# Performance work log

Measured on AMD Instinct MI355X. Metric: run time of the kernel, lower is better.

The kernel has to match this reference:

```python
import jax, jax.numpy as jnp
import numpy as np


def setup_inputs() -> dict:
    key = jax.random.key(0)
    kq, kk, kv = jax.random.split(key, 3)
    B, L, H, E = 4, 2048, 16, 64
    return {
        "queries": jax.random.normal(kq, (B, L, H, E), dtype=jnp.float32),
        "keys": jax.random.normal(kk, (B, L, H, E), dtype=jnp.float32),
        "values": jax.random.normal(kv, (B, L, H, E), dtype=jnp.float32),
    }


def reference(queries, keys, values):
    B, L, H, E = queries.shape
    S = keys.shape[1]
    scale = 1.0 / jnp.sqrt(jnp.asarray(E, queries.dtype))
    # scores: [B, H, L, S]
    scores = jnp.einsum("blhe,bshe->bhls", queries, keys)
    # causal mask: disallow s > l (upper triangle, diagonal=1)
    causal = jnp.triu(jnp.ones((L, S), dtype=bool), k=1)
    scores = jnp.where(causal[None, None], -jnp.inf, scores)
    A = jax.nn.softmax(scale * scores, axis=-1)
    V = jnp.einsum("bhls,bshd->blhd", A, values)
    return V
```

## Files before the change

### kernel.cpp

```cpp
#include <hip/hip_runtime.h>
#include <hip/hip_bf16.h>

typedef __attribute__((ext_vector_type(8))) short short8;
typedef __attribute__((ext_vector_type(4))) float f32x4;
typedef __attribute__((ext_vector_type(4))) float f4;
typedef __attribute__((ext_vector_type(2))) unsigned uint2v;
typedef __attribute__((ext_vector_type(4))) unsigned uint4v;

#define MFMA(a, b, c) __builtin_amdgcn_mfma_f32_16x16x32_bf16(a, b, c, 0, 0, 0)

constexpr int B_ = 4, L = 2048, H = 16, E = 64;
constexpr int QBLK = 128, KVBLK = 64, NW = 8;
constexpr int LDP = 72;
constexpr float LOG2E = 1.4426950408889634f;
constexpr float C2 = 14.426950408889634f;
constexpr size_t NELEM = (size_t)B_ * L * H * E;
constexpr size_t WS_NEEDED = NELEM * 2 * 2;
constexpr int TILE_SHORTS = KVBLK * E;

__device__ __forceinline__ unsigned short f2bf(float f) {
  union { float f; unsigned u; } x;
  x.f = f;
  unsigned r = x.u + 0x7fffu + ((x.u >> 16) & 1u);
  return (unsigned short)(r >> 16);
}

__device__ __forceinline__ float exp2_fast(float x) {
  float r;
  asm("v_exp_f32 %0, %1" : "=v"(r) : "v"(x));
  return r;
}
__device__ __forceinline__ unsigned cvt_pk_bf16(float lo, float hi) {
  unsigned r;
  asm("v_cvt_pk_bf16_f32 %0, %1, %2" : "=v"(r) : "v"(lo), "v"(hi));
  return r;
}

__device__ __forceinline__ void gload_lds16(const void* g, void* l) {
  __builtin_amdgcn_global_load_lds(
      (const __attribute__((address_space(1))) unsigned*)g,
      (__attribute__((address_space(3))) unsigned*)l, 16, 0, 0);
}

__device__ __forceinline__ void stage_tile8(const unsigned short* gtile,
                                            unsigned short* ltile,
                                            unsigned qb, unsigned qs) {
  gload_lds16((const char*)gtile + qs, (char*)ltile + qb);
}

__device__ __forceinline__ void barrier_fence() {
  asm volatile("" ::: "memory");
  __builtin_amdgcn_s_barrier();
  asm volatile("" ::: "memory");
}

__global__ __launch_bounds__(256)
void prep_all(const float* __restrict__ K, const float* __restrict__ V,
              unsigned short* __restrict__ Kb, unsigned short* __restrict__ Vt) {
  __shared__ unsigned short Ts[E][KVBLK + 8];
  const int tid = threadIdx.x;
  if (blockIdx.y == 0) {
    const size_t t = (size_t)blockIdx.x * 256 + tid;
    const size_t row = t >> 3;
    const int e0 = ((int)t & 7) * 8;
    const int h = (int)(row % H);
    const size_t bl = row / H;
    const int l = (int)(bl % L);
    const int b = (int)(bl / L);
    f4 a = *(const f4*)(K + t * 8);
    f4 c = *(const f4*)(K + t * 8 + 4);
    short8 o;
    o[0] = (short)f2bf(a[0]); o[1] = (short)f2bf(a[1]);
    o[2] = (short)f2bf(a[2]); o[3] = (short)f2bf(a[3]);
    o[4] = (short)f2bf(c[0]); o[5] = (short)f2bf(c[1]);
    o[6] = (short)f2bf(c[2]); o[7] = (short)f2bf(c[3]);
    *(short8*)(Kb + (((size_t)b * H + h) * L + l) * E + e0) = o;
    return;
  }
  const int blk = blockIdx.x;
  if (blk >= B_ * H * (L / KVBLK)) return;
  const int st = blk % (L / KVBLK);
  const int bh = blk / (L / KVBLK);
  const int h = bh % H, b = bh / H;
  const int r = tid >> 3, e0 = (tid & 7) * 8;
  const float* vp = V + (((size_t)b * L + st * KVBLK) * H + h) * E;
#pragma unroll
  for (int rr = 0; rr < 2; ++rr) {
    const int row = rr * 32 + r;
    f4 a = *(const f4*)(vp + (size_t)row * (H * E) + e0);
    f4 c = *(const f4*)(vp + (size_t)row * (H * E) + e0 + 4);
#pragma unroll
    for (int j = 0; j < 4; ++j) Ts[e0 + j][row] = f2bf(a[j]);
#pragma unroll
    for (int j = 0; j < 4; ++j) Ts[e0 + 4 + j][row] = f2bf(c[j]);
  }
  __syncthreads();
  const int e = tid >> 2, k0 = (tid & 3) * 16;
  unsigned short* op = Vt + ((size_t)bh * (L / KVBLK) + st) * (E * KVBLK) + e * KVBLK + k0;
  *(short8*)op = *(const short8*)&Ts[e][k0];
  *(short8*)(op + 8) = *(const short8*)&Ts[e][k0 + 8];
}

__global__ __launch_bounds__(512, 6)
void fattn3(const float* __restrict__ Q, const unsigned short* __restrict__ Kb,
            const unsigned short* __restrict__ Vt, float* __restrict__ O) {
  const int bh = blockIdx.x;
  const int qtile = (int)(gridDim.y - 1) - blockIdx.y;
  const int b = bh >> 4, h = bh & 15;
  const int tid = threadIdx.x;
  const int wid = tid >> 6;
  const int lane = tid & 63;
  const int lg = lane >> 4, lm = lane & 15;
  const int qrow0 = qtile * QBLK + wid * 16;

  __shared__ __align__(16) unsigned short Ks[2][TILE_SHORTS];
  __shared__ __align__(16) unsigned short Vs[2][TILE_SHORTS];
  __shared__ __align__(16) unsigned short Pt[NW][16 * LDP];

  const unsigned sqb = (unsigned)wid * 1024u + (unsigned)lane * 16u;
  const unsigned sqs = sqb ^ (((sqb >> 7) & 7u) << 4);

  const unsigned short* kbase = Kb + (size_t)bh * L * E;
  const unsigned short* vbase = Vt + (size_t)bh * L * E;

  stage_tile8(kbase, Ks[0], sqb, sqs);
  stage_tile8(vbase, Vs[0], sqb, sqs);

  int offA[4], offB[4];
#pragma unroll
  for (int ct = 0; ct < 4; ++ct) {
    const int row = ct * 16 + lm;
    offA[ct] = row * 128 + ((lg ^ (row & 7)) << 4);
    offB[ct] = row * 128 + (((4 + lg) ^ (row & 7)) << 4);
  }
  int wrOff[4];
#pragma unroll
  for (int ct = 0; ct < 4; ++ct) wrOff[ct] = (lm * LDP + ct * 16 + lg * 4) * 2;
  const int rdOff0 = (lm * LDP + lg * 8) * 2;
  const int rdOff1 = (lm * LDP + 32 + lg * 8) * 2;
  char* const ptw = (char*)Pt[wid];

  short8 qf0, qf1;
  {
    const float qsc = 0.125f * LOG2E;
    const float* qp = Q + (((size_t)b * L + qrow0 + lm) * H + h) * E + lg * 8;
    f4 a0 = *(const f4*)(qp);
    f4 a1 = *(const f4*)(qp + 4);
    f4 b0 = *(const f4*)(qp + 32);
    f4 b1 = *(const f4*)(qp + 36);
    uint4v u0 = { cvt_pk_bf16(a0[0] * qsc, a0[1] * qsc),
                  cvt_pk_bf16(a0[2] * qsc, a0[3] * qsc),
                  cvt_pk_bf16(a1[0] * qsc, a1[1] * qsc),
                  cvt_pk_bf16(a1[2] * qsc, a1[3] * qsc) };
    uint4v u1 = { cvt_pk_bf16(b0[0] * qsc, b0[1] * qsc),
                  cvt_pk_bf16(b0[2] * qsc, b0[3] * qsc),
                  cvt_pk_bf16(b1[0] * qsc, b1[1] * qsc),
                  cvt_pk_bf16(b1[2] * qsc, b1[3] * qsc) };
    qf0 = __builtin_bit_cast(short8, u0);
    qf1 = __builtin_bit_cast(short8, u1);
  }

  f32x4 o[4];
#pragma unroll
  for (int et = 0; et < 4; ++et) o[et] = (f32x4){0.f, 0.f, 0.f, 0.f};
  float lsum = 0.f;

  const int nkv = 2 * qtile + 2;
  const f32x4 cinit = (f32x4){-C2, -C2, -C2, -C2};

  for (int kt = 0; kt < nkv; ++kt) {
    const int cur = kt & 1, nxt = cur ^ 1;

    asm volatile("s_waitcnt lgkmcnt(0)" ::: "memory");
    barrier_fence();

    if (kt + 1 < nkv) {
      stage_tile8(kbase + (size_t)(kt + 1) * TILE_SHORTS, Ks[nxt], sqb, sqs);
      stage_tile8(vbase + (size_t)(kt + 1) * TILE_SHORTS, Vs[nxt], sqb, sqs);
      asm volatile("s_waitcnt vmcnt(2)" ::: "memory");
    } else {
      asm volatile("s_waitcnt vmcnt(0)" ::: "memory");
    }
    barrier_fence();

    const bool dead = (kt * KVBLK) > (qrow0 + 15);
    if (dead) continue;

    const char* kl = (const char*)Ks[cur];
    const char* vl = (const char*)Vs[cur];

    f32x4 stl[4];
    __builtin_amdgcn_s_setprio(1);
#pragma unroll
    for (int ct = 0; ct < 4; ++ct) {
      short8 k0f = *(const short8*)(kl + offA[ct]);
      short8 k1f = *(const short8*)(kl + offB[ct]);
      f32x4 acc = cinit;
      acc = MFMA(k0f, qf0, acc);
      acc = MFMA(k1f, qf1, acc);
      stl[ct] = acc;
    }
    __builtin_amdgcn_s_setprio(0);

    if (kt * KVBLK + KVBLK - 1 > qrow0) {
#pragma unroll
      for (int ct = 0; ct < 4; ++ct)
#pragma unroll
        for (int r = 0; r < 4; ++r) {
          const int key = kt * KVBLK + ct * 16 + lg * 4 + r;
          if (key > qrow0 + lm) stl[ct][r] = -1e30f;
        }
    }

#pragma unroll
    for (int ct = 0; ct < 4; ++ct)
#pragma unroll
      for (int r = 0; r < 4; ++r) {
        const float p = exp2_fast(stl[ct][r]);
        stl[ct][r] = p;
        lsum += p;
      }

#pragma unroll
    for (int ct = 0; ct < 4; ++ct) {
      uint2v w;
      w[0] = cvt_pk_bf16(stl[ct][0], stl[ct][1]);
      w[1] = cvt_pk_bf16(stl[ct][2], stl[ct][3]);
      *(uint2v*)(ptw + wrOff[ct]) = w;
    }
    short8 pf0 = *(const short8*)(ptw + rdOff0);
    short8 pf1 = *(const short8*)(ptw + rdOff1);

    __builtin_amdgcn_s_setprio(1);
#pragma unroll
    for (int et = 0; et < 4; ++et) {
      short8 v0 = *(const short8*)(vl + offA[et]);
      short8 v1 = *(const short8*)(vl + offB[et]);
      o[et] = MFMA(pf0, v0, o[et]);
      o[et] = MFMA(pf1, v1, o[et]);
    }
    __builtin_amdgcn_s_setprio(0);
  }

  lsum += __shfl_xor(lsum, 16);
  lsum += __shfl_xor(lsum, 32);
  float linv[4];
#pragma unroll
  for (int r = 0; r < 4; ++r) linv[r] = 1.f / __shfl(lsum, lg * 20 + r);
  float* op = O + (((size_t)b * L + qrow0 + lg * 4) * H + h) * E;
#pragma unroll
  for (int r = 0; r < 4; ++r)
#pragma unroll
    for (int et = 0; et < 4; ++et)
      op[(size_t)r * (H * E) + et * 16 + lm] = o[et][r] * linv[r];
}

constexpr int LDV_F = 72, LDP_F = 72;
__global__ __launch_bounds__(256, 2)
void fattn_v1(const float* __restrict__ Q, const float* __restrict__ K,
              const float* __restrict__ V, float* __restrict__ O) {
  const int qtile = blockIdx.x;
  const int bh = blockIdx.y;
  const int b = bh / H, h = bh % H;
  const int tid = threadIdx.x;
  const int wid = tid >> 6;
  const int lane = tid & 63;
  const int lg = lane >> 4, lm = lane & 15;
  __shared__ __align__(16) short Vs[E * LDV_F];
  __shared__ __align__(16) short Ps[4][16 * LDP_F];
  const int qrow0 = qtile * 64 + wid * 16;
  short8 qf[2];
  {
    const float* qp = Q + (((size_t)b * L + (qrow0 + lm)) * H + h) * E + lg * 8;
#pragma unroll
    for (int kc = 0; kc < 2; ++kc) {
      f4 a = *(const f4*)(qp + kc * 32);
      f4 c = *(const f4*)(qp + kc * 32 + 4);
      short8 r;
      r[0] = (short)f2bf(a[0] * 0.125f); r[1] = (short)f2bf(a[1] * 0.125f);
      r[2] = (short)f2bf(a[2] * 0.125f); r[3] = (short)f2bf(a[3] * 0.125f);
      r[4] = (short)f2bf(c[0] * 0.125f); r[5] = (short)f2bf(c[1] * 0.125f);
      r[6] = (short)f2bf(c[2] * 0.125f); r[7] = (short)f2bf(c[3] * 0.125f);
      qf[kc] = r;
    }
  }
  f32x4 o[4];
#pragma unroll
  for (int et = 0; et < 4; ++et) o[et] = (f32x4){0.f, 0.f, 0.f, 0.f};
  float mrow[4], lrow[4];
#pragma unroll
  for (int r = 0; r < 4; ++r) { mrow[r] = -1e30f; lrow[r] = 0.f; }
  const float* kbase = K + (((size_t)b * L) * H + h) * E;
  const float* vbase = V + (((size_t)b * L) * H + h) * E;
  const int nkv = qtile + 1;
  for (int kt = 0; kt < nkv; ++kt) {
    __syncthreads();
    {
      const int key = tid >> 2;
      const int eb = (tid & 3) * 16;
      const float* vp = vbase + (size_t)(kt * 64 + key) * (H * E) + eb;
#pragma unroll
      for (int i = 0; i < 4; ++i) {
        f4 v = *(const f4*)(vp + i * 4);
        Vs[(eb + i * 4 + 0) * LDV_F + key] = (short)f2bf(v[0]);
        Vs[(eb + i * 4 + 1) * LDV_F + key] = (short)f2bf(v[1]);
        Vs[(eb + i * 4 + 2) * LDV_F + key] = (short)f2bf(v[2]);
        Vs[(eb + i * 4 + 3) * LDV_F + key] = (short)f2bf(v[3]);
      }
    }
    f32x4 s[4];
#pragma unroll
    for (int ct = 0; ct < 4; ++ct) {
      f32x4 acc = (f32x4){0.f, 0.f, 0.f, 0.f};
      const float* kp = kbase + (size_t)(kt * 64 + ct * 16 + lm) * (H * E) + lg * 8;
#pragma unroll
      for (int kc = 0; kc < 2; ++kc) {
        f4 a = *(const f4*)(kp + kc * 32);
        f4 c = *(const f4*)(kp + kc * 32 + 4);
        short8 kf;
        kf[0] = (short)f2bf(a[0]); kf[1] = (short)f2bf(a[1]);
        kf[2] = (short)f2bf(a[2]); kf[3] = (short)f2bf(a[3]);
        kf[4] = (short)f2bf(c[0]); kf[5] = (short)f2bf(c[1]);
        kf[6] = (short)f2bf(c[2]); kf[7] = (short)f2bf(c[3]);
        acc = MFMA(qf[kc], kf, acc);
      }
      s[ct] = acc;
    }
    if (kt == nkv - 1) {
#pragma unroll
      for (int ct = 0; ct < 4; ++ct) {
        const int sg = kt * 64 + ct * 16 + lm;
#pragma unroll
        for (int r = 0; r < 4; ++r)
          if (sg > qrow0 + lg * 4 + r) s[ct][r] = -1e30f;
      }
    }
#pragma unroll
    for (int r = 0; r < 4; ++r) {
      float tm = fmaxf(fmaxf(s[0][r], s[1][r]), fmaxf(s[2][r], s[3][r]));
      tm = fmaxf(tm, __shfl_xor(tm, 1));
      tm = fmaxf(tm, __shfl_xor(tm, 2));
      tm = fmaxf(tm, __shfl_xor(tm, 4));
      tm = fmaxf(tm, __shfl_xor(tm, 8));
      const float mnew = fmaxf(mrow[r], tm);
      const float sc = __expf(mrow[r] - mnew);
      mrow[r] = mnew;
      float rs = 0.f;
#pragma unroll
      for (int ct = 0; ct < 4; ++ct) {
        const float p = __expf(s[ct][r] - mnew);
        s[ct][r] = p;
        rs += p;
      }
      rs += __shfl_xor(rs, 1);
      rs += __shfl_xor(rs, 2);
      rs += __shfl_xor(rs, 4);
      rs += __shfl_xor(rs, 8);
      lrow[r] = lrow[r] * sc + rs;
#pragma unroll
      for (int et = 0; et < 4; ++et) o[et][r] *= sc;
    }
#pragma unroll
    for (int ct = 0; ct < 4; ++ct)
#pragma unroll
      for (int r = 0; r < 4; ++r)
        Ps[wid][(lg * 4 + r) * LDP_F + ct * 16 + lm] = (short)f2bf(s[ct][r]);
    __syncthreads();
    short8 pf[2];
    pf[0] = *(const short8*)&Ps[wid][lm * LDP_F + 0 * 32 + lg * 8];
    pf[1] = *(const short8*)&Ps[wid][lm * LDP_F + 1 * 32 + lg * 8];
#pragma unroll
    for (int et = 0; et < 4; ++et)
#pragma unroll
      for (int kc = 0; kc < 2; ++kc) {
        short8 vf = *(const short8*)&Vs[(et * 16 + lm) * LDV_F + kc * 32 + lg * 8];
        o[et] = MFMA(pf[kc], vf, o[et]);
      }
  }
  float* op = O + (((size_t)b * L + qrow0) * H + h) * E;
#pragma unroll
  for (int r = 0; r < 4; ++r) {
    const float inv = 1.f / lrow[r];
#pragma unroll
    for (int et = 0; et < 4; ++et)
      op[(size_t)(lg * 4 + r) * (H * E) + et * 16 + lm] = o[et][r] * inv;
  }
}

extern "C" void kernel_launch(void* const* d_in, const int* in_sizes, int n_in,
                              void* d_out, int out_size, void* d_ws, size_t ws_size,
                              hipStream_t stream) {
  const float* Q = (const float*)d_in[0];
  const float* K = (const float*)d_in[1];
  const float* V = (const float*)d_in[2];
  float* Out = (float*)d_out;
  if (ws_size >= WS_NEEDED) {
    unsigned short* Kb = (unsigned short*)d_ws;
    unsigned short* Vt = Kb + NELEM;
    dim3 gp((unsigned)(NELEM / (256 * 8)), 2);
    prep_all<<<gp, 256, 0, stream>>>(K, V, Kb, Vt);
    dim3 grid(B_ * H, L / QBLK);
    fattn3<<<grid, 512, 0, stream>>>(Q, Kb, Vt, Out);
  } else {
    dim3 grid(L / 64, B_ * H);
    fattn_v1<<<grid, 256, 0, stream>>>(Q, K, V, Out);
  }
}
```

Measured before the change: 68.58 us.

## Rewrite flash attention kernel around 32x32x16 MFMA with register-resident P

Replaces the 16x16x32 MFMA attention kernel (8 waves, 16 query rows each) with a 4-wave kernel where each wave owns 32 query rows and uses 32x32x16 bf16 MFMAs for both QK^T and PV. The softmax probabilities are repacked into the B-operand layout with cross-half-wave shuffles instead of a round trip through per-wave LDS, which removes the P shared buffer. The aim is to raise MFMA efficiency, reuse each K/V fragment across more rows, and cut LDS traffic. In exchange each wave holds more accumulator registers, and there are fewer waves per block to hide latency.

```diff
diff --git a/kernel.cpp b/kernel.cpp
--- a/kernel.cpp
+++ b/kernel.cpp
@@ -2,16 +2,16 @@
 #include <hip/hip_bf16.h>
 
 typedef __attribute__((ext_vector_type(8))) short short8;
+typedef __attribute__((ext_vector_type(16))) float f32x16;
 typedef __attribute__((ext_vector_type(4))) float f32x4;
 typedef __attribute__((ext_vector_type(4))) float f4;
-typedef __attribute__((ext_vector_type(2))) unsigned uint2v;
 typedef __attribute__((ext_vector_type(4))) unsigned uint4v;
 
-#define MFMA(a, b, c) __builtin_amdgcn_mfma_f32_16x16x32_bf16(a, b, c, 0, 0, 0)
+#define MFMA16(a, b, c) __builtin_amdgcn_mfma_f32_16x16x32_bf16(a, b, c, 0, 0, 0)
+#define MFMA32(a, b, c) __builtin_amdgcn_mfma_f32_32x32x16_bf16(a, b, c, 0, 0, 0)
 
 constexpr int B_ = 4, L = 2048, H = 16, E = 64;
-constexpr int QBLK = 128, KVBLK = 64, NW = 8;
-constexpr int LDP = 72;
+constexpr int QBLK = 128, KVBLK = 64;
 constexpr float LOG2E = 1.4426950408889634f;
 constexpr float C2 = 14.426950408889634f;
 constexpr size_t NELEM = (size_t)B_ * L * H * E;
@@ -40,12 +40,6 @@
   __builtin_amdgcn_global_load_lds(
       (const __attribute__((address_space(1))) unsigned*)g,
       (__attribute__((address_space(3))) unsigned*)l, 16, 0, 0);
-}
-
-__device__ __forceinline__ void stage_tile8(const unsigned short* gtile,
-                                            unsigned short* ltile,
-                                            unsigned qb, unsigned qs) {
-  gload_lds16((const char*)gtile + qs, (char*)ltile + qb);
 }
 
 __device__ __forceinline__ void barrier_fence() {
@@ -101,72 +95,66 @@
   *(short8*)(op + 8) = *(const short8*)&Ts[e][k0 + 8];
 }
 
-__global__ __launch_bounds__(512, 6)
-void fattn3(const float* __restrict__ Q, const unsigned short* __restrict__ Kb,
-            const unsigned short* __restrict__ Vt, float* __restrict__ O) {
+__global__ __launch_bounds__(256, 4)
+void fattn32(const float* __restrict__ Q, const unsigned short* __restrict__ Kb,
+             const unsigned short* __restrict__ Vt, float* __restrict__ O) {
   const int bh = blockIdx.x;
   const int qtile = (int)(gridDim.y - 1) - blockIdx.y;
   const int b = bh >> 4, h = bh & 15;
   const int tid = threadIdx.x;
   const int wid = tid >> 6;
   const int lane = tid & 63;
-  const int lg = lane >> 4, lm = lane & 15;
-  const int qrow0 = qtile * QBLK + wid * 16;
+  const int ql = lane & 31;
+  const int hb = lane >> 5;
+  const int qw0 = qtile * QBLK + wid * 32;
+  const int qglob = qw0 + ql;
 
   __shared__ __align__(16) unsigned short Ks[2][TILE_SHORTS];
   __shared__ __align__(16) unsigned short Vs[2][TILE_SHORTS];
-  __shared__ __align__(16) unsigned short Pt[NW][16 * LDP];
-
-  const unsigned sqb = (unsigned)wid * 1024u + (unsigned)lane * 16u;
-  const unsigned sqs = sqb ^ (((sqb >> 7) & 7u) << 4);
+
+  const unsigned sb0 = (unsigned)wid * 2048u + (unsigned)lane * 16u;
+  const unsigned sb1 = sb0 + 1024u;
+  const unsigned ss0 = sb0 ^ (((sb0 >> 7) & 7u) << 4);
+  const unsigned ss1 = sb1 ^ (((sb1 >> 7) & 7u) << 4);
 
   const unsigned short* kbase = Kb + (size_t)bh * L * E;
   const unsigned short* vbase = Vt + (size_t)bh * L * E;
 
-  stage_tile8(kbase, Ks[0], sqb, sqs);
-  stage_tile8(vbase, Vs[0], sqb, sqs);
-
-  int offA[4], offB[4];
-#pragma unroll
-  for (int ct = 0; ct < 4; ++ct) {
-    const int row = ct * 16 + lm;
-    offA[ct] = row * 128 + ((lg ^ (row & 7)) << 4);
-    offB[ct] = row * 128 + (((4 + lg) ^ (row & 7)) << 4);
-  }
-  int wrOff[4];
-#pragma unroll
-  for (int ct = 0; ct < 4; ++ct) wrOff[ct] = (lm * LDP + ct * 16 + lg * 4) * 2;
-  const int rdOff0 = (lm * LDP + lg * 8) * 2;
-  const int rdOff1 = (lm * LDP + 32 + lg * 8) * 2;
-  char* const ptw = (char*)Pt[wid];
-
-  short8 qf0, qf1;
+  gload_lds16((const char*)kbase + ss0, (char*)Ks[0] + sb0);
+  gload_lds16((const char*)kbase + ss1, (char*)Ks[0] + sb1);
+  gload_lds16((const char*)vbase + ss0, (char*)Vs[0] + sb0);
+  gload_lds16((const char*)vbase + ss1, (char*)Vs[0] + sb1);
+
+  const int mq = ql & 7;
+  int off2[2][4];
+#pragma unroll
+  for (int t2 = 0; t2 < 2; ++t2)
+#pragma unroll
+    for (int j = 0; j < 4; ++j)
+      off2[t2][j] = (t2 * 32 + ql) * 128 + (((2 * j + hb) ^ mq) << 4);
+
+  short8 qf[4];
   {
     const float qsc = 0.125f * LOG2E;
-    const float* qp = Q + (((size_t)b * L + qrow0 + lm) * H + h) * E + lg * 8;
-    f4 a0 = *(const f4*)(qp);
-    f4 a1 = *(const f4*)(qp + 4);
-    f4 b0 = *(const f4*)(qp + 32);
-    f4 b1 = *(const f4*)(qp + 36);
-    uint4v u0 = { cvt_pk_bf16(a0[0] * qsc, a0[1] * qsc),
-                  cvt_pk_bf16(a0[2] * qsc, a0[3] * qsc),
-                  cvt_pk_bf16(a1[0] * qsc, a1[1] * qsc),
-                  cvt_pk_bf16(a1[2] * qsc, a1[3] * qsc) };
-    uint4v u1 = { cvt_pk_bf16(b0[0] * qsc, b0[1] * qsc),
-                  cvt_pk_bf16(b0[2] * qsc, b0[3] * qsc),
-                  cvt_pk_bf16(b1[0] * qsc, b1[1] * qsc),
-                  cvt_pk_bf16(b1[2] * qsc, b1[3] * qsc) };
-    qf0 = __builtin_bit_cast(short8, u0);
-    qf1 = __builtin_bit_cast(short8, u1);
-  }
-
-  f32x4 o[4];
-#pragma unroll
-  for (int et = 0; et < 4; ++et) o[et] = (f32x4){0.f, 0.f, 0.f, 0.f};
+    const float* qp = Q + (((size_t)b * L + qglob) * H + h) * E + hb * 8;
+#pragma unroll
+    for (int kc = 0; kc < 4; ++kc) {
+      f4 x0 = *(const f4*)(qp + kc * 16);
+      f4 x1 = *(const f4*)(qp + kc * 16 + 4);
+      uint4v u = { cvt_pk_bf16(x0[0] * qsc, x0[1] * qsc),
+                   cvt_pk_bf16(x0[2] * qsc, x0[3] * qsc),
+                   cvt_pk_bf16(x1[0] * qsc, x1[1] * qsc),
+                   cvt_pk_bf16(x1[2] * qsc, x1[3] * qsc) };
+      qf[kc] = __builtin_bit_cast(short8, u);
+    }
+  }
+
+  f32x16 o0, o1;
+#pragma unroll
+  for (int r = 0; r < 16; ++r) { o0[r] = 0.f; o1[r] = 0.f; }
   float lsum = 0.f;
 
   const int nkv = 2 * qtile + 2;
-  const f32x4 cinit = (f32x4){-C2, -C2, -C2, -C2};
 
   for (int kt = 0; kt < nkv; ++kt) {
     const int cur = kt & 1, nxt = cur ^ 1;
@@ -175,84 +163,94 @@
     barrier_fence();
 
     if (kt + 1 < nkv) {
-      stage_tile8(kbase + (size_t)(kt + 1) * TILE_SHORTS, Ks[nxt], sqb, sqs);
-      stage_tile8(vbase + (size_t)(kt + 1) * TILE_SHORTS, Vs[nxt], sqb, sqs);
-      asm volatile("s_waitcnt vmcnt(2)" ::: "memory");
+      const unsigned short* kg = kbase + (size_t)(kt + 1) * TILE_SHORTS;
+      const unsigned short* vg = vbase + (size_t)(kt + 1) * TILE_SHORTS;
+      gload_lds16((const char*)kg + ss0, (char*)Ks[nxt] + sb0);
+      gload_lds16((const char*)kg + ss1, (char*)Ks[nxt] + sb1);
+      gload_lds16((const char*)vg + ss0, (char*)Vs[nxt] + sb0);
+      gload_lds16((const char*)vg + ss1, (char*)Vs[nxt] + sb1);
+      asm volatile("s_waitcnt vmcnt(4)" ::: "memory");
     } else {
       asm volatile("s_waitcnt vmcnt(0)" ::: "memory");
     }
     barrier_fence();
 
-    const bool dead = (kt * KVBLK) > (qrow0 + 15);
+    const bool dead = (kt * KVBLK) > (qw0 + 31);
     if (dead) continue;
 
     const char* kl = (const char*)Ks[cur];
     const char* vl = (const char*)Vs[cur];
-
-    f32x4 stl[4];
-    __builtin_amdgcn_s_setprio(1);
-#pragma unroll
-    for (int ct = 0; ct < 4; ++ct) {
-      short8 k0f = *(const short8*)(kl + offA[ct]);
-      short8 k1f = *(const short8*)(kl + offB[ct]);
-      f32x4 acc = cinit;
-      acc = MFMA(k0f, qf0, acc);
-      acc = MFMA(k1f, qf1, acc);
-      stl[ct] = acc;
-    }
-    __builtin_amdgcn_s_setprio(0);
-
-    if (kt * KVBLK + KVBLK - 1 > qrow0) {
-#pragma unroll
-      for (int ct = 0; ct < 4; ++ct)
-#pragma unroll
-        for (int r = 0; r < 4; ++r) {
-          const int key = kt * KVBLK + ct * 16 + lg * 4 + r;
-          if (key > qrow0 + lm) stl[ct][r] = -1e30f;
+    const bool partial = (kt * KVBLK + KVBLK - 1) > qw0;
+
+#pragma unroll
+    for (int st = 0; st < 2; ++st) {
+      f32x16 sA;
+#pragma unroll
+      for (int r = 0; r < 16; ++r) sA[r] = -C2;
+      __builtin_amdgcn_s_setprio(1);
+#pragma unroll
+      for (int kc = 0; kc < 4; ++kc) {
+        short8 kf = *(const short8*)(kl + off2[st][kc]);
+        sA = MFMA32(kf, qf[kc], sA);
+      }
+      __builtin_amdgcn_s_setprio(0);
+
+      if (partial) {
+#pragma unroll
+        for (int r = 0; r < 16; ++r) {
+          const int key = kt * KVBLK + st * 32 + (r & 3) + 8 * (r >> 2) + 4 * hb;
+          if (key > qglob) sA[r] = -1e30f;
         }
-    }
-
-#pragma unroll
-    for (int ct = 0; ct < 4; ++ct)
-#pragma unroll
-      for (int r = 0; r < 4; ++r) {
-        const float p = exp2_fast(stl[ct][r]);
-        stl[ct][r] = p;
+      }
+
+#pragma unroll
+      for (int r = 0; r < 16; ++r) {
+        const float p = exp2_fast(sA[r]);
+        sA[r] = p;
         lsum += p;
       }
 
-#pragma unroll
-    for (int ct = 0; ct < 4; ++ct) {
-      uint2v w;
-      w[0] = cvt_pk_bf16(stl[ct][0], stl[ct][1]);
-      w[1] = cvt_pk_bf16(stl[ct][2], stl[ct][3]);
-      *(uint2v*)(ptw + wrOff[ct]) = w;
-    }
-    short8 pf0 = *(const short8*)(ptw + rdOff0);
-    short8 pf1 = *(const short8*)(ptw + rdOff1);
-
-    __builtin_amdgcn_s_setprio(1);
-#pragma unroll
-    for (int et = 0; et < 4; ++et) {
-      short8 v0 = *(const short8*)(vl + offA[et]);
-      short8 v1 = *(const short8*)(vl + offB[et]);
-      o[et] = MFMA(pf0, v0, o[et]);
-      o[et] = MFMA(pf1, v1, o[et]);
-    }
-    __builtin_amdgcn_s_setprio(0);
-  }
-
-  lsum += __shfl_xor(lsum, 16);
+      unsigned pk[8];
+#pragma unroll
+      for (int j = 0; j < 8; ++j) pk[j] = cvt_pk_bf16(sA[2 * j], sA[2 * j + 1]);
+      unsigned rc0 = __shfl_xor(hb ? pk[0] : pk[2], 32);
+      unsigned rc1 = __shfl_xor(hb ? pk[1] : pk[3], 32);
+      unsigned rc2 = __shfl_xor(hb ? pk[4] : pk[6], 32);
+      unsigned rc3 = __shfl_xor(hb ? pk[5] : pk[7], 32);
+      uint4v u0 = { hb ? rc0 : pk[0], hb ? rc1 : pk[1],
+                    hb ? pk[2] : rc0, hb ? pk[3] : rc1 };
+      uint4v u1 = { hb ? rc2 : pk[4], hb ? rc3 : pk[5],
+                    hb ? pk[6] : rc2, hb ? pk[7] : rc3 };
+      short8 pb0 = __builtin_bit_cast(short8, u0);
+      short8 pb1 = __builtin_bit_cast(short8, u1);
+
+      __builtin_amdgcn_s_setprio(1);
+      {
+        short8 v00 = *(const short8*)(vl + off2[0][2 * st]);
+        short8 v01 = *(const short8*)(vl + off2[0][2 * st + 1]);
+        short8 v10 = *(const short8*)(vl + off2[1][2 * st]);
+        short8 v11 = *(const short8*)(vl + off2[1][2 * st + 1]);
+        o0 = MFMA32(v00, pb0, o0);
+        o0 = MFMA32(v01, pb1, o0);
+        o1 = MFMA32(v10, pb0, o1);
+        o1 = MFMA32(v11, pb1, o1);
+      }
+      __builtin_amdgcn_s_setprio(0);
+    }
+  }
+
   lsum += __shfl_xor(lsum, 32);
-  float linv[4];
-#pragma unroll
-  for (int r = 0; r < 4; ++r) linv[r] = 1.f / __shfl(lsum, lg * 20 + r);
-  float* op = O + (((size_t)b * L + qrow0 + lg * 4) * H + h) * E;
-#pragma unroll
-  for (int r = 0; r < 4; ++r)
-#pragma unroll
-    for (int et = 0; et < 4; ++et)
-      op[(size_t)r * (H * E) + et * 16 + lm] = o[et][r] * linv[r];
+  const float linv = 1.f / lsum;
+  float* op = O + (((size_t)b * L + qglob) * H + h) * E;
+#pragma unroll
+  for (int qd = 0; qd < 4; ++qd) {
+    f4 v0 = { o0[4 * qd + 0] * linv, o0[4 * qd + 1] * linv,
+              o0[4 * qd + 2] * linv, o0[4 * qd + 3] * linv };
+    f4 v1 = { o1[4 * qd + 0] * linv, o1[4 * qd + 1] * linv,
+              o1[4 * qd + 2] * linv, o1[4 * qd + 3] * linv };
+    *(f4*)(op + qd * 8 + hb * 4) = v0;
+    *(f4*)(op + 32 + qd * 8 + hb * 4) = v1;
+  }
 }
 
 constexpr int LDV_F = 72, LDP_F = 72;
@@ -322,7 +320,7 @@
         kf[2] = (short)f2bf(a[2]); kf[3] = (short)f2bf(a[3]);
         kf[4] = (short)f2bf(c[0]); kf[5] = (short)f2bf(c[1]);
         kf[6] = (short)f2bf(c[2]); kf[7] = (short)f2bf(c[3]);
-        acc = MFMA(qf[kc], kf, acc);
+        acc = MFMA16(qf[kc], kf, acc);
       }
       s[ct] = acc;
     }
@@ -374,7 +372,7 @@
 #pragma unroll
       for (int kc = 0; kc < 2; ++kc) {
         short8 vf = *(const short8*)&Vs[(et * 16 + lm) * LDV_F + kc * 32 + lg * 8];
-        o[et] = MFMA(pf[kc], vf, o[et]);
+        o[et] = MFMA16(pf[kc], vf, o[et]);
       }
   }
   float* op = O + (((size_t)b * L + qrow0) * H + h) * E;
@@ -400,7 +398,7 @@
     dim3 gp((unsigned)(NELEM / (256 * 8)), 2);
     prep_all<<<gp, 256, 0, stream>>>(K, V, Kb, Vt);
     dim3 grid(B_ * H, L / QBLK);
-    fattn3<<<grid, 512, 0, stream>>>(Q, Kb, Vt, Out);
+    fattn32<<<grid, 256, 0, stream>>>(Q, Kb, Vt, Out);
   } else {
     dim3 grid(L / 64, B_ * H);
     fattn_v1<<<grid, 256, 0, stream>>>(Q, K, V, Out);
```

Result: slower. 75.10 us (+9.5%).
